# Optimization experiments

Measured on AMD Instinct MI355X. Metric: run time of the kernel, lower is better.

Reference implementation:

```python
import jax, jax.numpy as jnp
import numpy as np

B, DIM, H, W = 16, 512, 32, 32
C = 256          # internal channels = int(512*0.5)
HEADS = 4        # max(1, 256//64)
KD = 32          # key_dim = int(64*0.5)
HD = 64          # head_dim = 256//4
SCALE = KD ** -0.5


def _silu(x):
    return x * jax.nn.sigmoid(x)


def conv1x1(x, Wm, s, b, act):
    # 1x1 conv + folded eval-mode BN (scale/shift) + optional SiLU
    y = jnp.einsum('bchw,oc->bohw', x, Wm)
    y = y * s[None, :, None, None] + b[None, :, None, None]
    return _silu(y) if act else y


def dwconv3(x, Wd, s, b):
    # depthwise 3x3 conv (groups = channels) + BN scale/shift, no act
    y = jax.lax.conv_general_dilated(
        x, Wd, window_strides=(1, 1), padding='SAME',
        feature_group_count=x.shape[1],
        dimension_numbers=('NCHW', 'OIHW', 'NCHW'))
    return y * s[None, :, None, None] + b[None, :, None, None]


def _mk_conv(key, c_out, c_in, k=1):
    k1, k2, k3 = jax.random.split(key, 3)
    fan_in = c_in * k * k
    if k == 1:
        Wm = jax.random.normal(k1, (c_out, c_in), jnp.float32) * fan_in ** -0.5
    else:
        Wm = jax.random.normal(k1, (c_out, c_in, k, k), jnp.float32) * fan_in ** -0.5
    s = jax.random.uniform(k2, (c_out,), jnp.float32, 0.5, 1.5)
    b = 0.1 * jax.random.normal(k3, (c_out,), jnp.float32)
    return Wm, s, b


def setup_inputs() -> dict:
    key = jax.random.key(0)
    ks = jax.random.split(key, 8)
    x = jax.random.normal(ks[0], (B, DIM, H, W), jnp.float32)
    W_cv1, s_cv1, b_cv1 = _mk_conv(ks[1], 2 * C, DIM)
    W_qkv, s_qkv, b_qkv = _mk_conv(ks[2], C + 2 * HEADS * KD, C)  # 512 out
    W_proj, s_proj, b_proj = _mk_conv(ks[3], C, C)
    # depthwise 3x3: OIHW with I=1, groups=C
    W_pe, s_pe, b_pe = _mk_conv(ks[4], C, 1, k=3)
    W_ffn1, s_ffn1, b_ffn1 = _mk_conv(ks[5], 2 * C, C)
    W_ffn2, s_ffn2, b_ffn2 = _mk_conv(ks[6], C, 2 * C)
    W_cv2, s_cv2, b_cv2 = _mk_conv(ks[7], DIM, 2 * C)
    return {
        'x': x,
        'W_cv1': W_cv1, 's_cv1': s_cv1, 'b_cv1': b_cv1,
        'W_qkv': W_qkv, 's_qkv': s_qkv, 'b_qkv': b_qkv,
        'W_proj': W_proj, 's_proj': s_proj, 'b_proj': b_proj,
        'W_pe': W_pe, 's_pe': s_pe, 'b_pe': b_pe,
        'W_ffn1': W_ffn1, 's_ffn1': s_ffn1, 'b_ffn1': b_ffn1,
        'W_ffn2': W_ffn2, 's_ffn2': s_ffn2, 'b_ffn2': b_ffn2,
        'W_cv2': W_cv2, 's_cv2': s_cv2, 'b_cv2': b_cv2,
    }


def reference(x,
              W_cv1, s_cv1, b_cv1,
              W_qkv, s_qkv, b_qkv,
              W_proj, s_proj, b_proj,
              W_pe, s_pe, b_pe,
              W_ffn1, s_ffn1, b_ffn1,
              W_ffn2, s_ffn2, b_ffn2,
              W_cv2, s_cv2, b_cv2):
    bsz, _, h, w = x.shape
    n = h * w
    y = conv1x1(x, W_cv1, s_cv1, b_cv1, act=True)          # [b, 2C, h, w]
    a, bb = y[:, :C], y[:, C:]

    # ----- Attention on bb -----
    qkv = conv1x1(bb, W_qkv, s_qkv, b_qkv, act=False)       # [b, 2*h*kd + C, h, w]
    qkv = qkv.reshape(bsz, HEADS, 2 * KD + HD, n)
    q, k, v = qkv[:, :, :KD], qkv[:, :, KD:2 * KD], qkv[:, :, 2 * KD:]
    attn = jnp.einsum('bhdn,bhdm->bhnm', q, k) * SCALE      # [b, heads, n, n]
    attn = jax.nn.softmax(attn, axis=-1)
    xa = jnp.einsum('bhdm,bhnm->bhdn', v, attn).reshape(bsz, C, h, w)
    xa = xa + dwconv3(v.reshape(bsz, C, h, w), W_pe, s_pe, b_pe)
    xa = conv1x1(xa, W_proj, s_proj, b_proj, act=False)
    bb = bb + xa

    # ----- FFN on bb -----
    ff = conv1x1(bb, W_ffn1, s_ffn1, b_ffn1, act=True)
    ff = conv1x1(ff, W_ffn2, s_ffn2, b_ffn2, act=False)
    bb = bb + ff

    return conv1x1(jnp.concatenate([a, bb], axis=1), W_cv2, s_cv2, b_cv2, act=True)
```

## Files before the change

### kernel.cpp

```cpp
#include <hip/hip_runtime.h>

typedef unsigned short u16;
typedef __attribute__((ext_vector_type(8))) short short8;
typedef __attribute__((ext_vector_type(4))) float f32x4;
typedef __attribute__((ext_vector_type(4))) unsigned int uint4v;
typedef __attribute__((ext_vector_type(4))) unsigned short ushort4v;

#define N_PIX 1024
constexpr float SCALE = 0.17677669529663687f;

__device__ __forceinline__ float bf2f(u16 v) {
    unsigned u = ((unsigned)v) << 16;
    return __builtin_bit_cast(float, u);
}
__device__ __forceinline__ u16 f2bf(float f) {
    unsigned u = __builtin_bit_cast(unsigned, f);
    u += 0x7fff + ((u >> 16) & 1);
    return (u16)(u >> 16);
}
__device__ __forceinline__ float silu_f(float x) { return x / (1.f + __expf(-x)); }

__device__ __forceinline__ f32x4 mfma16(short8 a, short8 b, f32x4 c) {
    return __builtin_amdgcn_mfma_f32_16x16x32_bf16(a, b, c, 0, 0, 0);
}

__device__ __forceinline__ void gl_lds16(const u16* g, u16* l) {
    __builtin_amdgcn_global_load_lds(
        (const __attribute__((address_space(1))) unsigned int*)g,
        (__attribute__((address_space(3))) unsigned int*)l, 16, 0, 0);
}

__global__ void cvtw_k(const float* s0, u16* d0, int n0,
                       const float* s1, u16* d1, int n1,
                       const float* s2, u16* d2, int n2,
                       const float* s3, u16* d3, int n3,
                       const float* s4, u16* d4, int n4,
                       const float* s5, u16* d5, int n5)
{
    const float* sp = nullptr; u16* dp = nullptr; int n = 0;
    switch (blockIdx.y) {
        case 0: sp = s0; dp = d0; n = n0; break;
        case 1: sp = s1; dp = d1; n = n1; break;
        case 2: sp = s2; dp = d2; n = n2; break;
        case 3: sp = s3; dp = d3; n = n3; break;
        case 4: sp = s4; dp = d4; n = n4; break;
        case 5: sp = s5; dp = d5; n = n5; break;
    }
    for (int i = blockIdx.x * 256 + threadIdx.x; i < n; i += gridDim.x * 256)
        dp[i] = f2bf(sp[i]);
}

__global__ __launch_bounds__(256) void trans_k(const float* __restrict__ x, u16* __restrict__ xt)
{
    __shared__ float LT[64 * 65];
    const int tid = threadIdx.x;
    const int n0 = blockIdx.x * 64;
    const int c0 = blockIdx.y * 64;
    const int b  = blockIdx.z;
    const int w = tid >> 6, ln = tid & 63;
#pragma unroll
    for (int s = 0; s < 16; ++s) {
        int c = s * 4 + w;
        LT[c * 65 + ln] = x[((size_t)(b * 512 + c0 + c)) * N_PIX + n0 + ln];
    }
    __syncthreads();
#pragma unroll
    for (int s = 0; s < 16; ++s) {
        int n = s * 4 + w;
        xt[((size_t)(b * N_PIX + n0 + n)) * 512 + c0 + ln] = f2bf(LT[ln * 65 + n]);
    }
}

__global__ __launch_bounds__(256) void gemm_k(
    const u16* __restrict__ Xt, int xcs, int xcoff,
    const u16* __restrict__ Wb, int Cin,
    const float* __restrict__ sc, const float* __restrict__ bi,
    const u16* __restrict__ res, int rcs, int rcoff,
    u16* __restrict__ out, int ocs, int ocoff,
    float* __restrict__ out32,
    u16* __restrict__ vsep,
    int act)
{
    __shared__ __align__(16) u16 WT[2][128 * 32];
    __shared__ __align__(16) u16 XT[2][128 * 32];
    const int tid  = threadIdx.x;
    const int lane = tid & 63;
    const int w    = __builtin_amdgcn_readfirstlane(tid >> 6);
    const int wr = w >> 1, wc = w & 1;
    const int n0 = blockIdx.x * 128;
    const int o0 = blockIdx.y * 128;
    const int b  = blockIdx.z;
    const int l4 = lane >> 4, l15 = lane & 15;

    const int srow0 = w * 16 + (lane >> 2);
    const int srow1 = (w + 4) * 16 + (lane >> 2);
    const int skc   = (lane & 3) * 8;
    const u16* wg0 = Wb + (size_t)(o0 + srow0) * Cin + skc;
    const u16* wg1 = Wb + (size_t)(o0 + srow1) * Cin + skc;
    const u16* xg0 = Xt + ((size_t)(b * N_PIX + n0 + srow0)) * xcs + xcoff + skc;
    const u16* xg1 = Xt + ((size_t)(b * N_PIX + n0 + srow1)) * xcs + xcoff + skc;

    f32x4 acc[4][4];
#pragma unroll
    for (int i = 0; i < 4; ++i)
#pragma unroll
        for (int j = 0; j < 4; ++j) acc[i][j] = (f32x4){0.f, 0.f, 0.f, 0.f};

    const int nk = Cin >> 5;
    gl_lds16(wg0, &WT[0][w * 512]);
    gl_lds16(wg1, &WT[0][(w + 4) * 512]);
    gl_lds16(xg0, &XT[0][w * 512]);
    gl_lds16(xg1, &XT[0][(w + 4) * 512]);
    __syncthreads();

    for (int kk = 0; kk < nk; ++kk) {
        const int cur = kk & 1;
        if (kk + 1 < nk) {
            const int cc = (kk + 1) << 5;
            gl_lds16(wg0 + cc, &WT[cur ^ 1][w * 512]);
            gl_lds16(wg1 + cc, &WT[cur ^ 1][(w + 4) * 512]);
            gl_lds16(xg0 + cc, &XT[cur ^ 1][w * 512]);
            gl_lds16(xg1 + cc, &XT[cur ^ 1][(w + 4) * 512]);
        }
        short8 af[4], bfr[4];
#pragma unroll
        for (int i = 0; i < 4; ++i)
            af[i] = *(const short8*)&WT[cur][(wr * 64 + i * 16 + l15) * 32 + l4 * 8];
#pragma unroll
        for (int j = 0; j < 4; ++j)
            bfr[j] = *(const short8*)&XT[cur][(wc * 64 + j * 16 + l15) * 32 + l4 * 8];
#pragma unroll
        for (int i = 0; i < 4; ++i)
#pragma unroll
            for (int j = 0; j < 4; ++j)
                acc[i][j] = mfma16(af[i], bfr[j], acc[i][j]);
        __syncthreads();
    }

    const bool is_v = (vsep != nullptr) && (wr == 1);
#pragma unroll
    for (int i = 0; i < 4; ++i) {
        const int ob = o0 + wr * 64 + i * 16 + l4 * 4;
        float s4[4], b4[4];
#pragma unroll
        for (int r = 0; r < 4; ++r) { s4[r] = sc[ob + r]; b4[r] = bi[ob + r]; }
#pragma unroll
        for (int j = 0; j < 4; ++j) {
            const int n = n0 + wc * 64 + j * 16 + l15;
            float v[4];
#pragma unroll
            for (int r = 0; r < 4; ++r) {
                v[r] = acc[i][j][r] * s4[r] + b4[r];
                if (act) v[r] = silu_f(v[r]);
            }
            if (out32) {
                const int Cout = gridDim.y * 128;
#pragma unroll
                for (int r = 0; r < 4; ++r)
                    out32[((size_t)b * Cout + ob + r) * N_PIX + n] = v[r];
            } else if (is_v) {
                const int hh = ob >> 7;
                const int dv = (ob & 127) - 64;
                u16* vp = vsep + (((size_t)(b * 4 + hh)) * 64 + dv) * N_PIX + n;
#pragma unroll
                for (int r = 0; r < 4; ++r) vp[r * N_PIX] = f2bf(v[r]);
            } else {
                const size_t base = ((size_t)(b * N_PIX + n)) * ocs + ocoff + ob;
                if (res) {
                    ushort4v rr = *(const ushort4v*)&res[((size_t)(b * N_PIX + n)) * rcs + rcoff + ob];
#pragma unroll
                    for (int r = 0; r < 4; ++r) v[r] += bf2f(rr[r]);
                }
                ushort4v pk;
#pragma unroll
                for (int r = 0; r < 4; ++r) pk[r] = f2bf(v[r]);
                *(ushort4v*)&out[base] = pk;
            }
        }
    }
}

__global__ __launch_bounds__(256) void attn_k(
    const u16* __restrict__ qkvt, const u16* __restrict__ vsep,
    u16* __restrict__ xat)
{
    __shared__ __align__(16) u16 KT[2][64 * 40];
    __shared__ __align__(16) u16 VT[2][64 * 72];
    __shared__ __align__(16) u16 PL[4 * 16 * 72];
    const int tid  = threadIdx.x;
    const int lane = tid & 63;
    const int w    = __builtin_amdgcn_readfirstlane(tid >> 6);
    const int l4 = lane >> 4, l15 = lane & 15;
    const int h = blockIdx.y, b = blockIdx.z;
    const int n0w = blockIdx.x * 64 + w * 16;
    u16* PLw = PL + w * 16 * 72;

    const short8 qf = *(const short8*)&qkvt[((size_t)(b * N_PIX + n0w + l15)) * 512 + h * 128 + l4 * 8];

    const int skr = tid >> 2, skc = (tid & 3) * 8;
    const int svd = tid >> 3, svm = (tid & 7) * 8;
    const u16* kgbase = qkvt + ((size_t)(b * N_PIX + skr)) * 512 + h * 128 + 32 + skc;
    const u16* vgbase = vsep + (((size_t)(b * 4 + h)) * 64 + svd) * N_PIX + svm;

    float mrun[4], lrun[4];
#pragma unroll
    for (int r = 0; r < 4; ++r) { mrun[r] = -1e30f; lrun[r] = 0.f; }
    f32x4 accv[4];
#pragma unroll
    for (int d = 0; d < 4; ++d) accv[d] = (f32x4){0.f, 0.f, 0.f, 0.f};
    const f32x4 z4 = {0.f, 0.f, 0.f, 0.f};

    uint4v kreg = *(const uint4v*)(kgbase);
    uint4v vr0  = *(const uint4v*)(vgbase);
    uint4v vr1  = *(const uint4v*)(vgbase + 32 * N_PIX);

    for (int t = 0; t < 16; ++t) {
        const int cur = t & 1;
        *(uint4v*)&KT[cur][skr * 40 + skc] = kreg;
        *(uint4v*)&VT[cur][svd * 72 + svm] = vr0;
        *(uint4v*)&VT[cur][(svd + 32) * 72 + svm] = vr1;
        if (t < 15) {
            const int m1 = (t + 1) * 64;
            kreg = *(const uint4v*)(kgbase + (size_t)m1 * 512);
            vr0  = *(const uint4v*)(vgbase + m1);
            vr1  = *(const uint4v*)(vgbase + 32 * N_PIX + m1);
        }
        __syncthreads();

        f32x4 s[4];
        __builtin_amdgcn_s_setprio(1);
#pragma unroll
        for (int mt = 0; mt < 4; ++mt) {
            short8 kf = *(const short8*)&KT[cur][(mt * 16 + l15) * 40 + l4 * 8];
            s[mt] = mfma16(qf, kf, z4);
        }
        __builtin_amdgcn_s_setprio(0);

        float tm[4];
#pragma unroll
        for (int r = 0; r < 4; ++r) {
            float m_ = fmaxf(fmaxf(s[0][r], s[1][r]), fmaxf(s[2][r], s[3][r]));
            m_ = fmaxf(m_, __shfl_xor(m_, 1));
            m_ = fmaxf(m_, __shfl_xor(m_, 2));
            m_ = fmaxf(m_, __shfl_xor(m_, 4));
            m_ = fmaxf(m_, __shfl_xor(m_, 8));
            tm[r] = m_ * SCALE;
        }
#pragma unroll
        for (int r = 0; r < 4; ++r) {
            float mnew = fmaxf(mrun[r], tm[r]);
            float corr = __expf(mrun[r] - mnew);
            mrun[r] = mnew;
            lrun[r] *= corr;
#pragma unroll
            for (int d = 0; d < 4; ++d) accv[d][r] *= corr;
        }
#pragma unroll
        for (int mt = 0; mt < 4; ++mt)
#pragma unroll
            for (int r = 0; r < 4; ++r) {
                float p = __expf(s[mt][r] * SCALE - mrun[r]);
                lrun[r] += p;
                PLw[(l4 * 4 + r) * 72 + mt * 16 + l15] = f2bf(p);
            }

        __builtin_amdgcn_s_setprio(1);
#pragma unroll
        for (int mq = 0; mq < 2; ++mq) {
            short8 pa = *(const short8*)&PLw[l15 * 72 + mq * 32 + l4 * 8];
#pragma unroll
            for (int d = 0; d < 4; ++d) {
                short8 vf = *(const short8*)&VT[cur][(d * 16 + l15) * 72 + mq * 32 + l4 * 8];
                accv[d] = mfma16(pa, vf, accv[d]);
            }
        }
        __builtin_amdgcn_s_setprio(0);
    }

#pragma unroll
    for (int r = 0; r < 4; ++r) {
        float sum = lrun[r];
        sum += __shfl_xor(sum, 1);
        sum += __shfl_xor(sum, 2);
        sum += __shfl_xor(sum, 4);
        sum += __shfl_xor(sum, 8);
        lrun[r] = 1.f / sum;
    }
#pragma unroll
    for (int d = 0; d < 4; ++d)
#pragma unroll
        for (int r = 0; r < 4; ++r) {
            const int n = n0w + l4 * 4 + r;
            xat[((size_t)(b * N_PIX + n)) * 256 + h * 64 + d * 16 + l15] =
                f2bf(accv[d][r] * lrun[r]);
        }
}

__global__ __launch_bounds__(256) void pe_k(
    const u16* __restrict__ vsep, const float* __restrict__ Wpe,
    const float* __restrict__ spe, const float* __restrict__ bpe,
    u16* __restrict__ xat)
{
    const int t  = threadIdx.x;
    const int y0 = blockIdx.x * 2;
    const int b  = blockIdx.y;
    const u16* vp = vsep + ((size_t)(b * 256 + t)) * N_PIX;

    float rv[128];
#pragma unroll
    for (int rr = 0; rr < 4; ++rr) {
        const int yy = y0 - 1 + rr;
        if (yy >= 0 && yy < 32) {
#pragma unroll
            for (int g = 0; g < 4; ++g) {
                uint4v u = *(const uint4v*)&vp[yy * 32 + g * 8];
#pragma unroll
                for (int e = 0; e < 4; ++e) {
                    rv[rr * 32 + g * 8 + e * 2]     = bf2f((u16)(u[e] & 0xffff));
                    rv[rr * 32 + g * 8 + e * 2 + 1] = bf2f((u16)(u[e] >> 16));
                }
            }
        } else {
#pragma unroll
            for (int j = 0; j < 32; ++j) rv[rr * 32 + j] = 0.f;
        }
    }
    float w9[9];
#pragma unroll
    for (int i = 0; i < 9; ++i) w9[i] = Wpe[t * 9 + i];
    const float scv = spe[t], biv = bpe[t];
    u16* xp = xat + ((size_t)(b * N_PIX)) * 256 + t;

#pragma unroll
    for (int py = 0; py < 2; ++py)
#pragma unroll
        for (int px = 0; px < 32; ++px) {
            float a = 0.f;
#pragma unroll
            for (int ky = 0; ky < 3; ++ky) {
                const int lr = py + ky;
#pragma unroll
                for (int kx = 0; kx < 3; ++kx) {
                    const int xx = px + kx - 1;
                    if (xx >= 0 && xx < 32)
                        a = fmaf(w9[ky * 3 + kx], rv[lr * 32 + xx], a);
                }
            }
            const int n = (y0 + py) * 32 + px;
            u16* p = xp + (size_t)n * 256;
            *p = f2bf(bf2f(*p) + a * scv + biv);
        }
}

extern "C" void kernel_launch(void* const* d_in, const int* in_sizes, int n_in,
                              void* d_out, int out_size, void* d_ws, size_t ws_size,
                              hipStream_t stream)
{
    const float* x      = (const float*)d_in[0];
    const float* W_cv1  = (const float*)d_in[1];
    const float* s_cv1  = (const float*)d_in[2];
    const float* b_cv1  = (const float*)d_in[3];
    const float* W_qkv  = (const float*)d_in[4];
    const float* s_qkv  = (const float*)d_in[5];
    const float* b_qkv  = (const float*)d_in[6];
    const float* W_proj = (const float*)d_in[7];
    const float* s_proj = (const float*)d_in[8];
    const float* b_proj = (const float*)d_in[9];
    const float* W_pe   = (const float*)d_in[10];
    const float* s_pe   = (const float*)d_in[11];
    const float* b_pe   = (const float*)d_in[12];
    const float* W_ffn1 = (const float*)d_in[13];
    const float* s_ffn1 = (const float*)d_in[14];
    const float* b_ffn1 = (const float*)d_in[15];
    const float* W_ffn2 = (const float*)d_in[16];
    const float* s_ffn2 = (const float*)d_in[17];
    const float* b_ffn2 = (const float*)d_in[18];
    const float* W_cv2  = (const float*)d_in[19];
    const float* s_cv2  = (const float*)d_in[20];
    const float* b_cv2  = (const float*)d_in[21];

    u16* ws = (u16*)d_ws;
    u16* xt      = ws;
    u16* yt      = xt + 8388608;
    u16* qkvt    = yt + 8388608;
    u16* fft     = qkvt + 8388608;
    u16* vsep    = fft + 8388608;
    u16* xat     = vsep + 4194304;
    u16* wb_cv1  = xat + 4194304;
    u16* wb_qkv  = wb_cv1 + 262144;
    u16* wb_proj = wb_qkv + 131072;
    u16* wb_ffn1 = wb_proj + 65536;
    u16* wb_ffn2 = wb_ffn1 + 131072;
    u16* wb_cv2  = wb_ffn2 + 131072;

    cvtw_k<<<dim3(64, 6), 256, 0, stream>>>(
        W_cv1, wb_cv1, 512 * 512, W_qkv, wb_qkv, 512 * 256,
        W_proj, wb_proj, 256 * 256, W_ffn1, wb_ffn1, 512 * 256,
        W_ffn2, wb_ffn2, 256 * 512, W_cv2, wb_cv2, 512 * 512);
    trans_k<<<dim3(16, 8, 16), 256, 0, stream>>>(x, xt);

    gemm_k<<<dim3(8, 4, 16), 256, 0, stream>>>(
        xt, 512, 0, wb_cv1, 512, s_cv1, b_cv1,
        nullptr, 0, 0, yt, 512, 0, nullptr, nullptr, 1);
    gemm_k<<<dim3(8, 4, 16), 256, 0, stream>>>(
        yt, 512, 256, wb_qkv, 256, s_qkv, b_qkv,
        nullptr, 0, 0, qkvt, 512, 0, nullptr, vsep, 0);
    attn_k<<<dim3(16, 4, 16), 256, 0, stream>>>(qkvt, vsep, xat);
    pe_k<<<dim3(16, 16), 256, 0, stream>>>(vsep, W_pe, s_pe, b_pe, xat);
    gemm_k<<<dim3(8, 2, 16), 256, 0, stream>>>(
        xat, 256, 0, wb_proj, 256, s_proj, b_proj,
        yt, 512, 256, yt, 512, 256, nullptr, nullptr, 0);
    gemm_k<<<dim3(8, 4, 16), 256, 0, stream>>>(
        yt, 512, 256, wb_ffn1, 256, s_ffn1, b_ffn1,
        nullptr, 0, 0, fft, 512, 0, nullptr, nullptr, 1);
    gemm_k<<<dim3(8, 2, 16), 256, 0, stream>>>(
        fft, 512, 0, wb_ffn2, 512, s_ffn2, b_ffn2,
        yt, 512, 256, yt, 512, 256, nullptr, nullptr, 0);
    gemm_k<<<dim3(8, 4, 16), 256, 0, stream>>>(
        yt, 512, 0, wb_cv2, 512, s_cv2, b_cv2,
        nullptr, 0, 0, nullptr, 0, 0, (float*)d_out, nullptr, 1);
}
```

Measured before the change: 284.2 us.

## Use 8 waves per GEMM block and stage fp32 output through LDS

The 1x1-conv GEMM kernel moves from 4 waves to 8 waves per 128x128 tile. Each wave now computes a 32x64 sub-tile, which halves the accumulators per thread and gives one global-to-LDS load per thread per operand. The final fp32 output epilogue is rewritten to stage results through LDS in four 32-row chunks, so each thread writes contiguous 32-byte rows instead of scattered strided scalar stores. The cost is more LDS fragment reads per MFMA and extra barriers in the epilogue.

```diff
diff --git a/kernel.cpp b/kernel.cpp
--- a/kernel.cpp
+++ b/kernel.cpp
@@ -71,7 +71,7 @@
     }
 }
 
-__global__ __launch_bounds__(256) void gemm_k(
+__global__ __launch_bounds__(512) void gemm_k(
     const u16* __restrict__ Xt, int xcs, int xcoff,
     const u16* __restrict__ Wb, int Cin,
     const float* __restrict__ sc, const float* __restrict__ bi,
@@ -86,61 +86,86 @@
     const int tid  = threadIdx.x;
     const int lane = tid & 63;
     const int w    = __builtin_amdgcn_readfirstlane(tid >> 6);
-    const int wr = w >> 1, wc = w & 1;
+    const int wr = w & 3;
+    const int wc = w >> 2;
     const int n0 = blockIdx.x * 128;
     const int o0 = blockIdx.y * 128;
     const int b  = blockIdx.z;
     const int l4 = lane >> 4, l15 = lane & 15;
 
-    const int srow0 = w * 16 + (lane >> 2);
-    const int srow1 = (w + 4) * 16 + (lane >> 2);
-    const int skc   = (lane & 3) * 8;
-    const u16* wg0 = Wb + (size_t)(o0 + srow0) * Cin + skc;
-    const u16* wg1 = Wb + (size_t)(o0 + srow1) * Cin + skc;
-    const u16* xg0 = Xt + ((size_t)(b * N_PIX + n0 + srow0)) * xcs + xcoff + skc;
-    const u16* xg1 = Xt + ((size_t)(b * N_PIX + n0 + srow1)) * xcs + xcoff + skc;
-
-    f32x4 acc[4][4];
-#pragma unroll
-    for (int i = 0; i < 4; ++i)
+    const int srow = tid >> 2;
+    const int skc  = (tid & 3) * 8;
+    const u16* wg = Wb + (size_t)(o0 + srow) * Cin + skc;
+    const u16* xg = Xt + ((size_t)(b * N_PIX + n0 + srow)) * xcs + xcoff + skc;
+
+    f32x4 acc[2][4];
+#pragma unroll
+    for (int i = 0; i < 2; ++i)
 #pragma unroll
         for (int j = 0; j < 4; ++j) acc[i][j] = (f32x4){0.f, 0.f, 0.f, 0.f};
 
     const int nk = Cin >> 5;
-    gl_lds16(wg0, &WT[0][w * 512]);
-    gl_lds16(wg1, &WT[0][(w + 4) * 512]);
-    gl_lds16(xg0, &XT[0][w * 512]);
-    gl_lds16(xg1, &XT[0][(w + 4) * 512]);
+    gl_lds16(wg, &WT[0][tid * 8]);
+    gl_lds16(xg, &XT[0][tid * 8]);
     __syncthreads();
 
     for (int kk = 0; kk < nk; ++kk) {
         const int cur = kk & 1;
         if (kk + 1 < nk) {
             const int cc = (kk + 1) << 5;
-            gl_lds16(wg0 + cc, &WT[cur ^ 1][w * 512]);
-            gl_lds16(wg1 + cc, &WT[cur ^ 1][(w + 4) * 512]);
-            gl_lds16(xg0 + cc, &XT[cur ^ 1][w * 512]);
-            gl_lds16(xg1 + cc, &XT[cur ^ 1][(w + 4) * 512]);
-        }
-        short8 af[4], bfr[4];
-#pragma unroll
-        for (int i = 0; i < 4; ++i)
-            af[i] = *(const short8*)&WT[cur][(wr * 64 + i * 16 + l15) * 32 + l4 * 8];
+            gl_lds16(wg + cc, &WT[cur ^ 1][tid * 8]);
+            gl_lds16(xg + cc, &XT[cur ^ 1][tid * 8]);
+        }
+        short8 af[2], bfr[4];
+#pragma unroll
+        for (int i = 0; i < 2; ++i)
+            af[i] = *(const short8*)&WT[cur][(wr * 32 + i * 16 + l15) * 32 + l4 * 8];
 #pragma unroll
         for (int j = 0; j < 4; ++j)
             bfr[j] = *(const short8*)&XT[cur][(wc * 64 + j * 16 + l15) * 32 + l4 * 8];
 #pragma unroll
-        for (int i = 0; i < 4; ++i)
+        for (int i = 0; i < 2; ++i)
 #pragma unroll
             for (int j = 0; j < 4; ++j)
                 acc[i][j] = mfma16(af[i], bfr[j], acc[i][j]);
         __syncthreads();
     }
 
-    const bool is_v = (vsep != nullptr) && (wr == 1);
-#pragma unroll
-    for (int i = 0; i < 4; ++i) {
-        const int ob = o0 + wr * 64 + i * 16 + l4 * 4;
+    if (out32) {
+        const int Cout = gridDim.y * 128;
+        float* eplds = (float*)XT;
+        const int row = tid >> 4, cb = (tid & 15) * 8;
+#pragma unroll
+        for (int h = 0; h < 4; ++h) {
+            if (wr == h) {
+#pragma unroll
+                for (int i = 0; i < 2; ++i)
+#pragma unroll
+                    for (int j = 0; j < 4; ++j)
+#pragma unroll
+                        for (int r = 0; r < 4; ++r) {
+                            const int oo = i * 16 + l4 * 4 + r;
+                            const int go = o0 + h * 32 + oo;
+                            float v = acc[i][j][r] * sc[go] + bi[go];
+                            if (act) v = silu_f(v);
+                            eplds[oo * 128 + wc * 64 + j * 16 + l15] = v;
+                        }
+            }
+            __syncthreads();
+            const size_t gidx = ((size_t)b * Cout + o0 + h * 32 + row) * N_PIX + n0 + cb;
+            f32x4 a0 = *(const f32x4*)&eplds[row * 128 + cb];
+            f32x4 a1 = *(const f32x4*)&eplds[row * 128 + cb + 4];
+            *(f32x4*)&out32[gidx]     = a0;
+            *(f32x4*)&out32[gidx + 4] = a1;
+            __syncthreads();
+        }
+        return;
+    }
+
+    const bool is_v = (vsep != nullptr) && (wr >= 2);
+#pragma unroll
+    for (int i = 0; i < 2; ++i) {
+        const int ob = o0 + wr * 32 + i * 16 + l4 * 4;
         float s4[4], b4[4];
 #pragma unroll
         for (int r = 0; r < 4; ++r) { s4[r] = sc[ob + r]; b4[r] = bi[ob + r]; }
@@ -153,12 +178,7 @@
                 v[r] = acc[i][j][r] * s4[r] + b4[r];
                 if (act) v[r] = silu_f(v[r]);
             }
-            if (out32) {
-                const int Cout = gridDim.y * 128;
-#pragma unroll
-                for (int r = 0; r < 4; ++r)
-                    out32[((size_t)b * Cout + ob + r) * N_PIX + n] = v[r];
-            } else if (is_v) {
+            if (is_v) {
                 const int hh = ob >> 7;
                 const int dv = (ob & 127) - 64;
                 u16* vp = vsep + (((size_t)(b * 4 + hh)) * 64 + dv) * N_PIX + n;
@@ -399,24 +419,24 @@
         W_ffn2, wb_ffn2, 256 * 512, W_cv2, wb_cv2, 512 * 512);
     trans_k<<<dim3(16, 8, 16), 256, 0, stream>>>(x, xt);
 
-    gemm_k<<<dim3(8, 4, 16), 256, 0, stream>>>(
+    gemm_k<<<dim3(8, 4, 16), 512, 0, stream>>>(
         xt, 512, 0, wb_cv1, 512, s_cv1, b_cv1,
         nullptr, 0, 0, yt, 512, 0, nullptr, nullptr, 1);
-    gemm_k<<<dim3(8, 4, 16), 256, 0, stream>>>(
+    gemm_k<<<dim3(8, 4, 16), 512, 0, stream>>>(
         yt, 512, 256, wb_qkv, 256, s_qkv, b_qkv,
         nullptr, 0, 0, qkvt, 512, 0, nullptr, vsep, 0);
     attn_k<<<dim3(16, 4, 16), 256, 0, stream>>>(qkvt, vsep, xat);
     pe_k<<<dim3(16, 16), 256, 0, stream>>>(vsep, W_pe, s_pe, b_pe, xat);
-    gemm_k<<<dim3(8, 2, 16), 256, 0, stream>>>(
+    gemm_k<<<dim3(8, 2, 16), 512, 0, stream>>>(
         xat, 256, 0, wb_proj, 256, s_proj, b_proj,
         yt, 512, 256, yt, 512, 256, nullptr, nullptr, 0);
-    gemm_k<<<dim3(8, 4, 16), 256, 0, stream>>>(
+    gemm_k<<<dim3(8, 4, 16), 512, 0, stream>>>(
         yt, 512, 256, wb_ffn1, 256, s_ffn1, b_ffn1,
         nullptr, 0, 0, fft, 512, 0, nullptr, nullptr, 1);
-    gemm_k<<<dim3(8, 2, 16), 256, 0, stream>>>(
+    gemm_k<<<dim3(8, 2, 16), 512, 0, stream>>>(
         fft, 512, 0, wb_ffn2, 512, s_ffn2, b_ffn2,
         yt, 512, 256, yt, 512, 256, nullptr, nullptr, 0);
-    gemm_k<<<dim3(8, 4, 16), 256, 0, stream>>>(
+    gemm_k<<<dim3(8, 4, 16), 512, 0, stream>>>(
         yt, 512, 0, wb_cv2, 512, s_cv2, b_cv2,
         nullptr, 0, 0, nullptr, 0, 0, (float*)d_out, nullptr, 1);
 }
```

New measurement: 279.1 us. No clear change (-1.8%).
